# Performance work log

Hardware: AMD Instinct MI355X
Metric: run time of the kernel (lower is better)

Reference implementation:

```python
import jax, jax.numpy as jnp
import numpy as np

EMB = 1024
HID = 4 * EMB
HEADS = 16
HEAD_DIM = EMB // HEADS


def gelu_tanh(x):
    c = jnp.sqrt(jnp.asarray(2.0 / jnp.pi, x.dtype))
    return 0.5 * x * (1.0 + jnp.tanh(c * (x + 0.044715 * x ** 3)))


def layernorm(x, scale, shift, eps=1e-5):
    mean = jnp.mean(x, axis=-1, keepdims=True)
    var = jnp.var(x, axis=-1, keepdims=True)
    return scale * (x - mean) / jnp.sqrt(var + eps) + shift


def setup_inputs() -> dict:
    key = jax.random.key(0)
    ks = jax.random.split(key, 12)
    s = 0.02
    return {
        "x": jax.random.normal(ks[0], (2, 2048, EMB), jnp.float32),
        "Wq": jax.random.normal(ks[1], (EMB, EMB), jnp.float32) * s,
        "Wk": jax.random.normal(ks[2], (EMB, EMB), jnp.float32) * s,
        "Wv": jax.random.normal(ks[3], (EMB, EMB), jnp.float32) * s,
        "Wo": jax.random.normal(ks[4], (EMB, EMB), jnp.float32) * s,
        "bo": jnp.zeros((EMB,), jnp.float32),
        "W1": jax.random.normal(ks[5], (EMB, HID), jnp.float32) * s,
        "b1": jnp.zeros((HID,), jnp.float32),
        "W2": jax.random.normal(ks[6], (HID, EMB), jnp.float32) * s,
        "b2": jnp.zeros((EMB,), jnp.float32),
        "ln1_scale": jnp.ones((EMB,), jnp.float32),
        "ln1_shift": jnp.zeros((EMB,), jnp.float32),
        "ln2_scale": jnp.ones((EMB,), jnp.float32),
        "ln2_shift": jnp.zeros((EMB,), jnp.float32),
    }


def reference(x, Wq, Wk, Wv, Wo, bo, W1, b1, W2, b2,
              ln1_scale, ln1_shift, ln2_scale, ln2_shift):
    B, S, D = x.shape

    # pre-norm attention + residual
    h = layernorm(x, ln1_scale, ln1_shift)
    q = (h @ Wq).reshape(B, S, HEADS, HEAD_DIM).transpose(0, 2, 1, 3)  # bhsd
    k = (h @ Wk).reshape(B, S, HEADS, HEAD_DIM).transpose(0, 2, 1, 3)
    v = (h @ Wv).reshape(B, S, HEADS, HEAD_DIM).transpose(0, 2, 1, 3)

    scores = jnp.einsum("bhqd,bhkd->bhqk", q, k)
    causal = jnp.tril(jnp.ones((S, S), bool))
    scores = jnp.where(causal, scores, -jnp.inf)
    attn = jax.nn.softmax(scores / jnp.sqrt(jnp.asarray(HEAD_DIM, x.dtype)), axis=-1)
    ctx = jnp.einsum("bhqk,bhkd->bhqd", attn, v)
    ctx = ctx.transpose(0, 2, 1, 3).reshape(B, S, D)
    x = x + (ctx @ Wo + bo)

    # pre-norm FFN + residual
    h = layernorm(x, ln2_scale, ln2_shift)
    h = gelu_tanh(h @ W1 + b1) @ W2 + b2
    return x + h
```

## Files before the change

kernel.cpp:

```cpp
#include <hip/hip_runtime.h>
#include <hip/hip_bf16.h>
#include <stdint.h>

#define B_   2
#define S_   2048
#define D_   1024
#define H_   16
#define DH_  64
#define HID_ 4096
#define M_   4096

typedef __bf16 bf16x8 __attribute__((ext_vector_type(8)));
typedef float  f32x4  __attribute__((ext_vector_type(4)));
typedef float  f32x16 __attribute__((ext_vector_type(16)));
typedef uint32_t u32x4v __attribute__((ext_vector_type(4)));

typedef const uint32_t __attribute__((address_space(1))) u32g;
typedef uint32_t       __attribute__((address_space(3))) u32l;

#define SCL2K_ 0.18033688011112042f

__device__ __forceinline__ uint16_t f2bf(float f) {
  uint32_t u = __builtin_bit_cast(uint32_t, f);
  u += 0x7FFFu + ((u >> 16) & 1u);
  return (uint16_t)(u >> 16);
}

__device__ __forceinline__ float bf2f(uint16_t u) {
  return __builtin_bit_cast(float, (uint32_t)u << 16);
}

__device__ __forceinline__ void gload_lds16(const void* g, void* l) {
  __builtin_amdgcn_global_load_lds((u32g*)g, (u32l*)l, 16, 0, 0);
}

__device__ __forceinline__ const bf16x8* lds8p(const uint16_t* base, int row,
                                               int cole) {
  int byt = (cole * 2) ^ ((row & 7) << 4);
  return reinterpret_cast<const bf16x8*>(base + row * 64 + (byt >> 1));
}

__device__ __forceinline__ const bf16x8* lds8p32(const uint16_t* base, int row,
                                                 int cole) {
  int byt = (cole * 2) ^ ((row & 7) << 4) ^ ((row & 8) << 2);
  return reinterpret_cast<const bf16x8*>(base + row * 64 + (byt >> 1));
}

__device__ __forceinline__ uint32_t cvtpk_bf16(float lo, float hi) {
  uint32_t d;
  asm("v_cvt_pk_bf16_f32 %0, %1, %2" : "=v"(d) : "v"(lo), "v"(hi));
  return d;
}
__device__ __forceinline__ void pl32swap(uint32_t& a, uint32_t& b) {
  asm volatile("v_permlane32_swap_b32 %0, %1" : "+v"(a), "+v"(b));
}

__global__ void wconv_all(const float* __restrict__ Wq, const float* __restrict__ Wk,
                          const float* __restrict__ Wv, const float* __restrict__ Wo,
                          const float* __restrict__ W1, const float* __restrict__ W2,
                          uint16_t* __restrict__ WQKVT, uint16_t* __restrict__ WOT,
                          uint16_t* __restrict__ W1T, uint16_t* __restrict__ W2T) {
  __shared__ float tile[32][33];
  int idx = blockIdx.x;
  const float* W;
  uint16_t* WT;
  int K, N, within;
  if (idx < 4096) {
    int which = idx >> 10;
    within = idx & 1023;
    W = (which == 0) ? Wq : (which == 1) ? Wk : (which == 2) ? Wv : Wo;
    WT = (which == 3) ? WOT : WQKVT + (size_t)which * 1024 * 1024;
    K = 1024; N = 1024;
  } else if (idx < 8192) {
    within = idx - 4096; W = W1; WT = W1T; K = 1024; N = 4096;
  } else {
    within = idx - 8192; W = W2; WT = W2T; K = 4096; N = 1024;
  }
  int nb = N >> 5;
  int n0 = (within % nb) * 32, k0 = (within / nb) * 32;
  int tx = threadIdx.x, ty = threadIdx.y;
#pragma unroll
  for (int i = 0; i < 4; ++i)
    tile[ty + i * 8][tx] = W[(size_t)(k0 + ty + i * 8) * N + n0 + tx];
  __syncthreads();
#pragma unroll
  for (int i = 0; i < 4; ++i)
    WT[(size_t)(n0 + ty + i * 8) * K + k0 + tx] = f2bf(tile[tx][ty + i * 8]);
}

__global__ __launch_bounds__(256) void ln_k(const float* __restrict__ x,
                                            const float* __restrict__ sc,
                                            const float* __restrict__ sh,
                                            uint16_t* __restrict__ out) {
  int row = blockIdx.x;
  int t = threadIdx.x;
  float4 v = reinterpret_cast<const float4*>(x + (size_t)row * D_)[t];
  float s = v.x + v.y + v.z + v.w;
  float ss = v.x * v.x + v.y * v.y + v.z * v.z + v.w * v.w;
#pragma unroll
  for (int off = 32; off >= 1; off >>= 1) {
    s += __shfl_xor(s, off);
    ss += __shfl_xor(ss, off);
  }
  __shared__ float red[8];
  int wid = t >> 6, lane = t & 63;
  if (lane == 0) { red[wid] = s; red[wid + 4] = ss; }
  __syncthreads();
  s = red[0] + red[1] + red[2] + red[3];
  ss = red[4] + red[5] + red[6] + red[7];
  float mean = s * (1.0f / D_);
  float var = ss * (1.0f / D_) - mean * mean;
  float rstd = rsqrtf(var + 1e-5f);
  float4 g = reinterpret_cast<const float4*>(sc)[t];
  float4 b = reinterpret_cast<const float4*>(sh)[t];
  ushort4 o;
  o.x = f2bf(g.x * (v.x - mean) * rstd + b.x);
  o.y = f2bf(g.y * (v.y - mean) * rstd + b.y);
  o.z = f2bf(g.z * (v.z - mean) * rstd + b.z);
  o.w = f2bf(g.w * (v.w - mean) * rstd + b.w);
  reinterpret_cast<ushort4*>(out + (size_t)row * D_)[t] = o;
}

__global__ __launch_bounds__(256) void reduce4_k(
    const uint16_t* __restrict__ P0, const uint16_t* __restrict__ P1,
    const uint16_t* __restrict__ P2, const uint16_t* __restrict__ P3,
    const float* __restrict__ resid, const float* __restrict__ bias,
    float* __restrict__ out) {
  int row = blockIdx.x, t = threadIdx.x;
  size_t base = (size_t)row * D_ + t * 4;
  float4 r = *reinterpret_cast<const float4*>(resid + base);
  float4 b = reinterpret_cast<const float4*>(bias)[t];
  ushort4 u0 = *reinterpret_cast<const ushort4*>(P0 + base);
  ushort4 u1 = *reinterpret_cast<const ushort4*>(P1 + base);
  ushort4 u2 = *reinterpret_cast<const ushort4*>(P2 + base);
  ushort4 u3 = *reinterpret_cast<const ushort4*>(P3 + base);
  float4 o;
  o.x = r.x + b.x + bf2f(u0.x) + bf2f(u1.x) + bf2f(u2.x) + bf2f(u3.x);
  o.y = r.y + b.y + bf2f(u0.y) + bf2f(u1.y) + bf2f(u2.y) + bf2f(u3.y);
  o.z = r.z + b.z + bf2f(u0.z) + bf2f(u1.z) + bf2f(u2.z) + bf2f(u3.z);
  o.w = r.w + b.w + bf2f(u0.w) + bf2f(u1.w) + bf2f(u2.w) + bf2f(u3.w);
  *reinterpret_cast<float4*>(out + base) = o;
}

__global__ void vtrans_k(const uint16_t* __restrict__ V, uint16_t* __restrict__ VT) {
  __shared__ uint16_t tile[32][33];
  int s0 = blockIdx.x * 32, d0 = blockIdx.y * 32, bh = blockIdx.z;
  int tx = threadIdx.x, ty = threadIdx.y;
  const uint16_t* vb = V + (size_t)bh * S_ * DH_;
  uint16_t* vtb = VT + (size_t)bh * DH_ * S_;
#pragma unroll
  for (int i = 0; i < 4; ++i)
    tile[ty + i * 8][tx] = vb[(size_t)(s0 + ty + i * 8) * DH_ + d0 + tx];
  __syncthreads();
#pragma unroll
  for (int i = 0; i < 4; ++i)
    vtb[(size_t)(d0 + ty + i * 8) * S_ + s0 + tx] = tile[tx][ty + i * 8];
}

template <int EPI>
__global__ __launch_bounds__(512, 2) void gemm8(
    const uint16_t* __restrict__ A, const uint16_t* __restrict__ BT,
    void* __restrict__ Cout, const float* __restrict__ bias,
    uint16_t* __restrict__ P0, uint16_t* __restrict__ P1,
    uint16_t* __restrict__ P2, uint16_t* __restrict__ P3,
    int M, int N, int K) {
  __shared__ uint16_t As[2][2][128 * 64];
  __shared__ uint16_t Bs[2][2][128 * 64];
  int t = threadIdx.x;
  int lane = t & 63, wid = t >> 6;
  int wm = wid >> 2, wn = wid & 3;
  int l15 = lane & 15, lk8 = (lane >> 4) * 8, lr4 = (lane >> 4) * 4;
  int gx = gridDim.x;
  int nwg = gx * gridDim.y;
  int bid = blockIdx.y * gx + blockIdx.x;
  int swz = (bid & 7) * (nwg >> 3) + (bid >> 3);
  int bx = swz % gx, by = swz / gx;
  int m0 = by * 256, n0 = bx * 256;
  int ksz = K / gridDim.z;
  int kbeg = blockIdx.z * ksz;
  int NT = ksz >> 6;

  int r0 = t >> 3, slot0 = t & 7;
  int scol = (slot0 ^ (r0 & 7)) * 8;

  auto STAGE_A = [&](int kt, int half, int buf) {
    const uint16_t* src =
        A + (size_t)(m0 + half * 128 + r0) * K + kbeg + kt * 64 + scol;
    uint16_t* dst = &As[buf][half][t * 8];
    gload_lds16(src, dst);
    gload_lds16(src + (size_t)64 * K, dst + 4096);
  };
  auto STAGE_B = [&](int kt, int half, int buf) {
    const uint16_t* src =
        BT + (size_t)(n0 + half * 128 + r0) * K + kbeg + kt * 64 + scol;
    uint16_t* dst = &Bs[buf][half][t * 8];
    gload_lds16(src, dst);
    gload_lds16(src + (size_t)64 * K, dst + 4096);
  };

  bf16x8 a[4][2], b[2][2];
  auto LDA = [&](int buf, int mh) {
#pragma unroll
    for (int j = 0; j < 4; ++j)
#pragma unroll
      for (int kk = 0; kk < 2; ++kk)
        a[j][kk] = *lds8p(As[buf][mh], wm * 64 + j * 16 + l15, kk * 32 + lk8);
  };
  auto LDB = [&](int buf, int nh) {
#pragma unroll
    for (int jj = 0; jj < 2; ++jj)
#pragma unroll
      for (int kk = 0; kk < 2; ++kk)
        b[jj][kk] = *lds8p(Bs[buf][nh], wn * 32 + jj * 16 + l15, kk * 32 + lk8);
  };

  f32x4 acc[8][4] = {};
  auto MM = [&](int mh, int nh) {
    __builtin_amdgcn_s_setprio(1);
#pragma unroll
    for (int kk = 0; kk < 2; ++kk)
#pragma unroll
      for (int j = 0; j < 4; ++j)
#pragma unroll
        for (int jj = 0; jj < 2; ++jj)
          acc[mh * 4 + j][nh * 2 + jj] = __builtin_amdgcn_mfma_f32_16x16x32_bf16(
              a[j][kk], b[jj][kk], acc[mh * 4 + j][nh * 2 + jj], 0, 0, 0);
    __builtin_amdgcn_s_setprio(0);
  };
  auto BAR = [&]() {
    __builtin_amdgcn_s_barrier();
    asm volatile("" ::: "memory");
  };
  auto LGKM0 = [&]() {
    asm volatile("s_waitcnt lgkmcnt(0)" ::: "memory");
    __builtin_amdgcn_sched_barrier(0);
  };

  STAGE_A(0, 0, 0);
  STAGE_B(0, 1, 0);
  STAGE_B(0, 0, 0);
  STAGE_A(0, 1, 0);
  STAGE_A(1, 0, 1);
  STAGE_B(1, 1, 1);
  asm volatile("s_waitcnt vmcnt(4)" ::: "memory");
  BAR();

  for (int T = 0; T < NT; ++T) {
    int cur = T & 1;
    LDA(cur, 0);
    LDB(cur, 0);
    if (T + 1 < NT) STAGE_B(T + 1, 0, cur ^ 1);
    BAR(); LGKM0();
    MM(0, 0);
    BAR();
    LDB(cur, 1);
    if (T + 1 < NT) STAGE_A(T + 1, 1, cur ^ 1);
    BAR(); LGKM0();
    MM(0, 1);
    BAR();
    LDA(cur, 1);
    if (T + 2 < NT) STAGE_A(T + 2, 0, cur);
    BAR(); LGKM0();
    MM(1, 1);
    BAR();
    LDB(cur, 0);
    if (T + 2 < NT) STAGE_B(T + 2, 1, cur);
    BAR(); LGKM0();
    MM(1, 0);
    if (T + 1 < NT) {
      if (T == NT - 2) {
        asm volatile("s_waitcnt vmcnt(0)" ::: "memory");
      } else {
        asm volatile("s_waitcnt vmcnt(4)" ::: "memory");
      }
    }
    BAR();
  }

  uint16_t* Pz = nullptr;
  if constexpr (EPI == 3) {
    int z = blockIdx.z;
    Pz = (z == 0) ? P0 : (z == 1) ? P1 : (z == 2) ? P2 : P3;
  }
#pragma unroll
  for (int mi = 0; mi < 8; ++mi) {
#pragma unroll
    for (int ni = 0; ni < 4; ++ni) {
#pragma unroll
      for (int rr = 0; rr < 4; ++rr) {
        int gm = m0 + (mi >> 2) * 128 + wm * 64 + (mi & 3) * 16 + lr4 + rr;
        int gn = n0 + (ni >> 1) * 128 + wn * 32 + (ni & 1) * 16 + l15;
        float v = acc[mi][ni][rr];
        if constexpr (EPI == 0) {
          int which = gn >> 10, nc = gn & 1023;
          int h = nc >> 6, dh = nc & 63;
          int bb = gm >> 11, s = gm & 2047;
          if (which == 1) v *= SCL2K_;
          ((uint16_t*)Cout)[((size_t)which * 32 + bb * 16 + h) * (S_ * 64) +
                            (size_t)s * 64 + dh] = f2bf(v);
        } else if constexpr (EPI == 2) {
          float u = v + bias[gn];
          float y = 0.7978845608028654f * (u + 0.044715f * u * u * u);
          float e = __expf(2.0f * y);
          float th = 1.0f - 2.0f / (e + 1.0f);
          ((uint16_t*)Cout)[(size_t)gm * N + gn] = f2bf(0.5f * u * (1.0f + th));
        } else {
          Pz[(size_t)gm * N + gn] = f2bf(v);
        }
      }
    }
  }
}

template <int EPI>
__global__ __launch_bounds__(256) void gemm_bt(
    const uint16_t* __restrict__ A, const uint16_t* __restrict__ BT,
    void* __restrict__ Cout, const float* __restrict__ bias,
    const float* __restrict__ resid, int M, int N, int K) {
  __shared__ uint16_t Asm_[128 * 64];
  __shared__ uint16_t Bsm_[128 * 64];
  int t = threadIdx.x;
  int lane = t & 63, wid = t >> 6;
  int wr = wid >> 1, wc = wid & 1;
  int nwg = gridDim.x * gridDim.y;
  int bid = blockIdx.y * gridDim.x + blockIdx.x;
  int swz = (bid & 7) * (nwg >> 3) + (bid >> 3);
  int bx = swz % gridDim.x, by = swz / gridDim.x;
  int m0 = by * 128, n0 = bx * 128;
  int l15 = lane & 15, lk8 = (lane >> 4) * 8;
  f32x4 acc[4][4] = {};

  auto STAGE = [&](int k0) {
#pragma unroll
    for (int it = 0; it < 4; ++it) {
      int idx = it * 256 + t;
      int r = idx >> 3, slot = idx & 7;
      int c = (slot ^ (r & 7)) * 8;
      gload_lds16(A + (size_t)(m0 + r) * K + k0 + c, &Asm_[idx * 8]);
      gload_lds16(BT + (size_t)(n0 + r) * K + k0 + c, &Bsm_[idx * 8]);
    }
  };

  int niter = K >> 6;
  for (int ki = 0; ki < niter; ++ki) {
    __syncthreads();
    STAGE(ki * 64);
    __syncthreads();
#pragma unroll
    for (int kk = 0; kk < 2; ++kk) {
      bf16x8 a[4], b[4];
#pragma unroll
      for (int mi = 0; mi < 4; ++mi)
        a[mi] = *lds8p(Asm_, wr * 64 + mi * 16 + l15, kk * 32 + lk8);
#pragma unroll
      for (int ni = 0; ni < 4; ++ni)
        b[ni] = *lds8p(Bsm_, wc * 64 + ni * 16 + l15, kk * 32 + lk8);
#pragma unroll
      for (int mi = 0; mi < 4; ++mi)
#pragma unroll
        for (int ni = 0; ni < 4; ++ni)
          acc[mi][ni] = __builtin_amdgcn_mfma_f32_16x16x32_bf16(
              a[mi], b[ni], acc[mi][ni], 0, 0, 0);
    }
  }
  int lr4 = (lane >> 4) * 4;
#pragma unroll
  for (int mi = 0; mi < 4; ++mi) {
#pragma unroll
    for (int ni = 0; ni < 4; ++ni) {
#pragma unroll
      for (int r = 0; r < 4; ++r) {
        int gm = m0 + wr * 64 + mi * 16 + lr4 + r;
        int gn = n0 + wc * 64 + ni * 16 + l15;
        float v = acc[mi][ni][r];
        if constexpr (EPI == 1) {
          ((float*)Cout)[(size_t)gm * N + gn] =
              resid[(size_t)gm * N + gn] + v + bias[gn];
        }
      }
    }
  }
}

__global__ __launch_bounds__(64) void attn32s_k(const uint16_t* __restrict__ Q,
                                                const uint16_t* __restrict__ Kv,
                                                const uint16_t* __restrict__ VT,
                                                uint16_t* __restrict__ Obuf,
                                                float* __restrict__ ML) {
  __shared__ uint16_t Ksm[2][32 * 64];
  __shared__ uint16_t Vsm[2][32 * 64];
  int bid = blockIdx.x;
  int bh = bid & 31;
  int s = (bid >> 5) & 1;
  int qt = bid >> 6;
  int lane = threadIdx.x;
  int l31 = lane & 31, lh = lane >> 5;
  int nkt = qt + 1;
  int h = (nkt + 1) >> 1;
  int t0 = s ? h : 0, t1 = s ? nkt : h;
  int pb = ((qt * 32 + bh) << 1) + s;

  f32x16 o0 = {}, o1 = {};
  float mrow = -3.0e38f, lsum = 0.0f;

  auto STAGE = [&](int k0, int bufi) {
#pragma unroll
    for (int c = 0; c < 4; ++c) {
      int idx = c * 64 + lane;
      int r = idx >> 3, sl = idx & 7;
      int slp = sl ^ (r & 7) ^ ((r & 8) >> 2);
      gload_lds16(Kv + ((size_t)bh * S_ + k0 + r) * 64 + slp * 8,
                  &Ksm[bufi][idx * 8]);
      int dh = 2 * r + (slp >> 2), ko = (slp & 3) * 8;
      gload_lds16(VT + ((size_t)bh * 64 + dh) * S_ + k0 + ko,
                  &Vsm[bufi][idx * 8]);
    }
  };

  if (t0 < t1) {
    int qbase = qt * 32;
    bf16x8 qf[4];
#pragma unroll
    for (int dk = 0; dk < 4; ++dk)
      qf[dk] = *reinterpret_cast<const bf16x8*>(
          Q + ((size_t)bh * S_ + qbase + l31) * 64 + dk * 16 + lh * 8);

    int buf = 0;
    STAGE(t0 * 32, 0);
    for (int t = t0; t < t1; ++t) {
      if (t + 1 < t1) {
        STAGE((t + 1) * 32, buf ^ 1);
        asm volatile("s_waitcnt vmcnt(8)" ::: "memory");
      } else {
        asm volatile("s_waitcnt vmcnt(0)" ::: "memory");
      }
      __builtin_amdgcn_sched_barrier(0);
      f32x16 Sf = {};
#pragma unroll
      for (int dk = 0; dk < 4; ++dk) {
        bf16x8 kf = *lds8p32(Ksm[buf], l31, dk * 16 + lh * 8);
        Sf = __builtin_amdgcn_mfma_f32_32x32x16_bf16(kf, qf[dk], Sf, 0, 0, 0);
      }
      float sv[16];
      if (t == qt) {
#pragma unroll
        for (int rr = 0; rr < 16; ++rr) {
          int koff = (rr & 3) + 8 * (rr >> 2) + 4 * lh;
          sv[rr] = (koff <= l31) ? Sf[rr] : -3.0e38f;
        }
      } else {
#pragma unroll
        for (int rr = 0; rr < 16; ++rr) sv[rr] = Sf[rr];
      }
      float mt16 = sv[0];
#pragma unroll
      for (int rr = 1; rr < 16; ++rr) mt16 = fmaxf(mt16, sv[rr]);
      if (__any(mt16 > mrow + 8.0f)) {
        float mt = mt16;
#pragma unroll
        for (int off = 32; off >= 1; off >>= 1)
          mt = fmaxf(mt, __shfl_xor(mt, off));
        mt = fmaxf(mt, mrow);
        float fac = __builtin_amdgcn_exp2f(mrow - mt);
        mrow = mt;
        lsum *= fac;
#pragma unroll
        for (int rr = 0; rr < 16; ++rr) { o0[rr] *= fac; o1[rr] *= fac; }
      }
      float pv[16];
#pragma unroll
      for (int rr = 0; rr < 16; ++rr) {
        pv[rr] = __builtin_amdgcn_exp2f(sv[rr] - mrow);
        lsum += pv[rr];
      }
      uint32_t a0 = cvtpk_bf16(pv[0], pv[1]), b0 = cvtpk_bf16(pv[4], pv[5]);
      pl32swap(a0, b0);
      uint32_t a1 = cvtpk_bf16(pv[2], pv[3]), b1 = cvtpk_bf16(pv[6], pv[7]);
      pl32swap(a1, b1);
      u32x4v w0 = {a0, a1, b0, b1};
      bf16x8 pa0 = __builtin_bit_cast(bf16x8, w0);
      uint32_t a2 = cvtpk_bf16(pv[8], pv[9]), b2 = cvtpk_bf16(pv[12], pv[13]);
      pl32swap(a2, b2);
      uint32_t a3 = cvtpk_bf16(pv[10], pv[11]), b3 = cvtpk_bf16(pv[14], pv[15]);
      pl32swap(a3, b3);
      u32x4v w1 = {a2, a3, b2, b3};
      bf16x8 pa1 = __builtin_bit_cast(bf16x8, w1);
      int vrow = l31 >> 1, vcb = (l31 & 1) * 32 + lh * 8;
      bf16x8 v00 = *lds8p32(Vsm[buf], vrow, vcb);
      o0 = __builtin_amdgcn_mfma_f32_32x32x16_bf16(pa0, v00, o0, 0, 0, 0);
      bf16x8 v01 = *lds8p32(Vsm[buf], vrow, vcb + 16);
      o0 = __builtin_amdgcn_mfma_f32_32x32x16_bf16(pa1, v01, o0, 0, 0, 0);
      bf16x8 v10 = *lds8p32(Vsm[buf], 16 + vrow, vcb);
      o1 = __builtin_amdgcn_mfma_f32_32x32x16_bf16(pa0, v10, o1, 0, 0, 0);
      bf16x8 v11 = *lds8p32(Vsm[buf], 16 + vrow, vcb + 16);
      o1 = __builtin_amdgcn_mfma_f32_32x32x16_bf16(pa1, v11, o1, 0, 0, 0);
      buf ^= 1;
    }
    lsum += __shfl_xor(lsum, 32);
  }

  if (lane < 32) {
    ML[(size_t)pb * 64 + l31 * 2] = mrow;
    ML[(size_t)pb * 64 + l31 * 2 + 1] = lsum;
  }
#pragma unroll
  for (int rr = 0; rr < 16; ++rr) {
    int srow = (rr & 3) + 8 * (rr >> 2) + 4 * lh;
    size_t base = (size_t)pb * 2048 + srow * 64;
    Obuf[base + l31] = f2bf(o0[rr]);
    Obuf[base + 32 + l31] = f2bf(o1[rr]);
  }
}

__global__ __launch_bounds__(64) void attncomb_k(const uint16_t* __restrict__ Obuf,
                                                 const float* __restrict__ ML,
                                                 uint16_t* __restrict__ ctx) {
  int blk = blockIdx.x;
  int qt = blk >> 5, bh = blk & 31;
  int lane = threadIdx.x;
  int q = lane >> 1, half = lane & 1;
  size_t pb0 = (size_t)blk * 2, pb1 = pb0 + 1;
  float m0 = ML[pb0 * 64 + q * 2], l0 = ML[pb0 * 64 + q * 2 + 1];
  float m1 = ML[pb1 * 64 + q * 2], l1 = ML[pb1 * 64 + q * 2 + 1];
  float m = fmaxf(m0, m1);
  float w0 = __builtin_amdgcn_exp2f(m0 - m), w1 = __builtin_amdgcn_exp2f(m1 - m);
  float invL = 1.0f / (l0 * w0 + l1 * w1);
  int b_ = bh >> 4, h_ = bh & 15;
  int srow = qt * 32 + q;
  size_t ib = pb0 * 2048 + q * 64 + half * 32;
  size_t ob = ((size_t)(b_ * S_ + srow)) * D_ + h_ * 64 + half * 32;
#pragma unroll
  for (int i = 0; i < 8; ++i) {
    ushort4 u0 = *reinterpret_cast<const ushort4*>(Obuf + ib + i * 4);
    ushort4 u1 = *reinterpret_cast<const ushort4*>(Obuf + 2048 + ib + i * 4);
    ushort4 o;
    o.x = f2bf((bf2f(u0.x) * w0 + bf2f(u1.x) * w1) * invL);
    o.y = f2bf((bf2f(u0.y) * w0 + bf2f(u1.y) * w1) * invL);
    o.z = f2bf((bf2f(u0.z) * w0 + bf2f(u1.z) * w1) * invL);
    o.w = f2bf((bf2f(u0.w) * w0 + bf2f(u1.w) * w1) * invL);
    *reinterpret_cast<ushort4*>(ctx + ob + i * 4) = o;
  }
}

extern "C" void kernel_launch(void* const* d_in, const int* in_sizes, int n_in,
                              void* d_out, int out_size, void* d_ws, size_t ws_size,
                              hipStream_t stream) {
  const float* x    = (const float*)d_in[0];
  const float* Wq   = (const float*)d_in[1];
  const float* Wk   = (const float*)d_in[2];
  const float* Wv   = (const float*)d_in[3];
  const float* Wo   = (const float*)d_in[4];
  const float* bo   = (const float*)d_in[5];
  const float* W1   = (const float*)d_in[6];
  const float* b1   = (const float*)d_in[7];
  const float* W2   = (const float*)d_in[8];
  const float* b2   = (const float*)d_in[9];
  const float* ln1s = (const float*)d_in[10];
  const float* ln1b = (const float*)d_in[11];
  const float* ln2s = (const float*)d_in[12];
  const float* ln2b = (const float*)d_in[13];
  float* out = (float*)d_out;
  char* ws = (char*)d_ws;

  const size_t MB = 1024 * 1024;
  uint16_t* WQKVT = (uint16_t*)(ws + 0);
  uint16_t* WOT   = (uint16_t*)(ws + 6 * MB);
  uint16_t* W1T   = (uint16_t*)(ws + 8 * MB);
  uint16_t* W2T   = (uint16_t*)(ws + 16 * MB);
  uint16_t* H1    = (uint16_t*)(ws + 24 * MB);
  float*    X1    = (float*)(ws + 32 * MB);
  uint16_t* QKV   = (uint16_t*)(ws + 48 * MB);
  uint16_t* VTb   = (uint16_t*)(ws + 72 * MB);
  uint16_t* CTX   = (uint16_t*)(ws + 80 * MB);
  uint16_t* FFH   = (uint16_t*)(ws + 48 * MB);
  uint16_t* AOB   = (uint16_t*)(ws + 24 * MB);
  float*    AML   = (float*)(ws + 40 * MB);
  uint16_t* SP0   = (uint16_t*)(ws + 0);
  uint16_t* SP1   = (uint16_t*)(ws + 8 * MB);
  uint16_t* SP2   = (uint16_t*)(ws + 24 * MB);
  uint16_t* SP3   = (uint16_t*)(ws + 80 * MB);

  dim3 b32x8(32, 8);
  wconv_all<<<dim3(12288), b32x8, 0, stream>>>(Wq, Wk, Wv, Wo, W1, W2,
                                               WQKVT, WOT, W1T, W2T);
  ln_k<<<M_, 256, 0, stream>>>(x, ln1s, ln1b, H1);
  gemm8<0><<<dim3(12, 16), 512, 0, stream>>>(H1, WQKVT, QKV, nullptr,
                                             nullptr, nullptr, nullptr, nullptr,
                                             M_, 3072, 1024);
  const uint16_t* Qp = QKV;
  const uint16_t* Kp = QKV + (size_t)32 * S_ * 64;
  const uint16_t* Vp = QKV + (size_t)64 * S_ * 64;
  vtrans_k<<<dim3(64, 2, 32), b32x8, 0, stream>>>(Vp, VTb);
  attn32s_k<<<dim3(4096), 64, 0, stream>>>(Qp, Kp, VTb, AOB, AML);
  attncomb_k<<<dim3(2048), 64, 0, stream>>>(AOB, AML, CTX);
  gemm_bt<1><<<dim3(8, 32), 256, 0, stream>>>(CTX, WOT, X1, bo, x, M_, 1024, 1024);
  ln_k<<<M_, 256, 0, stream>>>(X1, ln2s, ln2b, H1);
  gemm8<2><<<dim3(16, 16), 512, 0, stream>>>(H1, W1T, FFH, b1,
                                             nullptr, nullptr, nullptr, nullptr,
                                             M_, 4096, 1024);
  gemm8<3><<<dim3(4, 16, 4), 512, 0, stream>>>(FFH, W2T, nullptr, nullptr,
                                               SP0, SP1, SP2, SP3,
                                               M_, 1024, 4096);
  reduce4_k<<<M_, 256, 0, stream>>>(SP0, SP1, SP2, SP3, X1, b2, out);
}
```

Before: 245.8 us.

## Split attention KV range three ways, schedule heavy tiles first, fuse LN1 into weight prep

The attention kernel now splits each query tile's causal key range into three chunks instead of two, and launches the longest query tiles first to improve load balance. The combine kernel merges three partial results. The first layernorm is folded into the weight conversion kernel to save a launch. s_setprio is raised around the MFMA sections. AML is moved to workspace offset 0, which risks overlapping other buffers, and a three-way split adds more partial-output traffic.

```diff
diff --git a/kernel.cpp b/kernel.cpp
--- a/kernel.cpp
+++ b/kernel.cpp
@@ -55,13 +55,46 @@
   asm volatile("v_permlane32_swap_b32 %0, %1" : "+v"(a), "+v"(b));
 }
 
-__global__ void wconv_all(const float* __restrict__ Wq, const float* __restrict__ Wk,
-                          const float* __restrict__ Wv, const float* __restrict__ Wo,
-                          const float* __restrict__ W1, const float* __restrict__ W2,
-                          uint16_t* __restrict__ WQKVT, uint16_t* __restrict__ WOT,
-                          uint16_t* __restrict__ W1T, uint16_t* __restrict__ W2T) {
+__global__ void prep_k(const float* __restrict__ Wq, const float* __restrict__ Wk,
+                       const float* __restrict__ Wv, const float* __restrict__ Wo,
+                       const float* __restrict__ W1, const float* __restrict__ W2,
+                       uint16_t* __restrict__ WQKVT, uint16_t* __restrict__ WOT,
+                       uint16_t* __restrict__ W1T, uint16_t* __restrict__ W2T,
+                       const float* __restrict__ x, const float* __restrict__ sc,
+                       const float* __restrict__ sh, uint16_t* __restrict__ lnout) {
+  int idx = blockIdx.x;
+  int tx = threadIdx.x, ty = threadIdx.y;
+  if (idx >= 12288) {
+    int row = idx - 12288;
+    int t = ty * 32 + tx;
+    float4 v = reinterpret_cast<const float4*>(x + (size_t)row * D_)[t];
+    float s = v.x + v.y + v.z + v.w;
+    float ss = v.x * v.x + v.y * v.y + v.z * v.z + v.w * v.w;
+#pragma unroll
+    for (int off = 32; off >= 1; off >>= 1) {
+      s += __shfl_xor(s, off);
+      ss += __shfl_xor(ss, off);
+    }
+    __shared__ float red[8];
+    int wid = t >> 6, lane = t & 63;
+    if (lane == 0) { red[wid] = s; red[wid + 4] = ss; }
+    __syncthreads();
+    s = red[0] + red[1] + red[2] + red[3];
+    ss = red[4] + red[5] + red[6] + red[7];
+    float mean = s * (1.0f / D_);
+    float var = ss * (1.0f / D_) - mean * mean;
+    float rstd = rsqrtf(var + 1e-5f);
+    float4 g = reinterpret_cast<const float4*>(sc)[t];
+    float4 b = reinterpret_cast<const float4*>(sh)[t];
+    ushort4 o;
+    o.x = f2bf(g.x * (v.x - mean) * rstd + b.x);
+    o.y = f2bf(g.y * (v.y - mean) * rstd + b.y);
+    o.z = f2bf(g.z * (v.z - mean) * rstd + b.z);
+    o.w = f2bf(g.w * (v.w - mean) * rstd + b.w);
+    reinterpret_cast<ushort4*>(lnout + (size_t)row * D_)[t] = o;
+    return;
+  }
   __shared__ float tile[32][33];
-  int idx = blockIdx.x;
   const float* W;
   uint16_t* WT;
   int K, N, within;
@@ -78,7 +111,6 @@
   }
   int nb = N >> 5;
   int n0 = (within % nb) * 32, k0 = (within / nb) * 32;
-  int tx = threadIdx.x, ty = threadIdx.y;
 #pragma unroll
   for (int i = 0; i < 4; ++i)
     tile[ty + i * 8][tx] = W[(size_t)(k0 + ty + i * 8) * N + n0 + tx];
@@ -391,14 +423,14 @@
   __shared__ uint16_t Vsm[2][32 * 64];
   int bid = blockIdx.x;
   int bh = bid & 31;
-  int s = (bid >> 5) & 1;
-  int qt = bid >> 6;
+  int s = (bid >> 5) % 3;
+  int qt = 63 - bid / 96;
   int lane = threadIdx.x;
   int l31 = lane & 31, lh = lane >> 5;
   int nkt = qt + 1;
-  int h = (nkt + 1) >> 1;
-  int t0 = s ? h : 0, t1 = s ? nkt : h;
-  int pb = ((qt * 32 + bh) << 1) + s;
+  int chunk = (nkt + 2) / 3;
+  int t0 = s * chunk, t1 = min(nkt, t0 + chunk);
+  int pb = (qt * 32 + bh) * 3 + s;
 
   f32x16 o0 = {}, o1 = {};
   float mrow = -3.0e38f, lsum = 0.0f;
@@ -436,11 +468,13 @@
       }
       __builtin_amdgcn_sched_barrier(0);
       f32x16 Sf = {};
+      __builtin_amdgcn_s_setprio(1);
 #pragma unroll
       for (int dk = 0; dk < 4; ++dk) {
         bf16x8 kf = *lds8p32(Ksm[buf], l31, dk * 16 + lh * 8);
         Sf = __builtin_amdgcn_mfma_f32_32x32x16_bf16(kf, qf[dk], Sf, 0, 0, 0);
       }
+      __builtin_amdgcn_s_setprio(0);
       float sv[16];
       if (t == qt) {
 #pragma unroll
@@ -486,6 +520,7 @@
       u32x4v w1 = {a2, a3, b2, b3};
       bf16x8 pa1 = __builtin_bit_cast(bf16x8, w1);
       int vrow = l31 >> 1, vcb = (l31 & 1) * 32 + lh * 8;
+      __builtin_amdgcn_s_setprio(1);
       bf16x8 v00 = *lds8p32(Vsm[buf], vrow, vcb);
       o0 = __builtin_amdgcn_mfma_f32_32x32x16_bf16(pa0, v00, o0, 0, 0, 0);
       bf16x8 v01 = *lds8p32(Vsm[buf], vrow, vcb + 16);
@@ -494,6 +529,7 @@
       o1 = __builtin_amdgcn_mfma_f32_32x32x16_bf16(pa0, v10, o1, 0, 0, 0);
       bf16x8 v11 = *lds8p32(Vsm[buf], 16 + vrow, vcb + 16);
       o1 = __builtin_amdgcn_mfma_f32_32x32x16_bf16(pa1, v11, o1, 0, 0, 0);
+      __builtin_amdgcn_s_setprio(0);
       buf ^= 1;
     }
     lsum += __shfl_xor(lsum, 32);
@@ -519,12 +555,15 @@
   int qt = blk >> 5, bh = blk & 31;
   int lane = threadIdx.x;
   int q = lane >> 1, half = lane & 1;
-  size_t pb0 = (size_t)blk * 2, pb1 = pb0 + 1;
+  size_t pb0 = (size_t)blk * 3;
   float m0 = ML[pb0 * 64 + q * 2], l0 = ML[pb0 * 64 + q * 2 + 1];
-  float m1 = ML[pb1 * 64 + q * 2], l1 = ML[pb1 * 64 + q * 2 + 1];
-  float m = fmaxf(m0, m1);
-  float w0 = __builtin_amdgcn_exp2f(m0 - m), w1 = __builtin_amdgcn_exp2f(m1 - m);
-  float invL = 1.0f / (l0 * w0 + l1 * w1);
+  float m1 = ML[(pb0 + 1) * 64 + q * 2], l1 = ML[(pb0 + 1) * 64 + q * 2 + 1];
+  float m2 = ML[(pb0 + 2) * 64 + q * 2], l2 = ML[(pb0 + 2) * 64 + q * 2 + 1];
+  float m = fmaxf(fmaxf(m0, m1), m2);
+  float w0 = __builtin_amdgcn_exp2f(m0 - m);
+  float w1 = __builtin_amdgcn_exp2f(m1 - m);
+  float w2 = __builtin_amdgcn_exp2f(m2 - m);
+  float invL = 1.0f / (l0 * w0 + l1 * w1 + l2 * w2);
   int b_ = bh >> 4, h_ = bh & 15;
   int srow = qt * 32 + q;
   size_t ib = pb0 * 2048 + q * 64 + half * 32;
@@ -533,11 +572,12 @@
   for (int i = 0; i < 8; ++i) {
     ushort4 u0 = *reinterpret_cast<const ushort4*>(Obuf + ib + i * 4);
     ushort4 u1 = *reinterpret_cast<const ushort4*>(Obuf + 2048 + ib + i * 4);
+    ushort4 u2 = *reinterpret_cast<const ushort4*>(Obuf + 4096 + ib + i * 4);
     ushort4 o;
-    o.x = f2bf((bf2f(u0.x) * w0 + bf2f(u1.x) * w1) * invL);
-    o.y = f2bf((bf2f(u0.y) * w0 + bf2f(u1.y) * w1) * invL);
-    o.z = f2bf((bf2f(u0.z) * w0 + bf2f(u1.z) * w1) * invL);
-    o.w = f2bf((bf2f(u0.w) * w0 + bf2f(u1.w) * w1) * invL);
+    o.x = f2bf((bf2f(u0.x) * w0 + bf2f(u1.x) * w1 + bf2f(u2.x) * w2) * invL);
+    o.y = f2bf((bf2f(u0.y) * w0 + bf2f(u1.y) * w1 + bf2f(u2.y) * w2) * invL);
+    o.z = f2bf((bf2f(u0.z) * w0 + bf2f(u1.z) * w1 + bf2f(u2.z) * w2) * invL);
+    o.w = f2bf((bf2f(u0.w) * w0 + bf2f(u1.w) * w1 + bf2f(u2.w) * w2) * invL);
     *reinterpret_cast<ushort4*>(ctx + ob + i * 4) = o;
   }
 }
@@ -574,16 +614,16 @@
   uint16_t* CTX   = (uint16_t*)(ws + 80 * MB);
   uint16_t* FFH   = (uint16_t*)(ws + 48 * MB);
   uint16_t* AOB   = (uint16_t*)(ws + 24 * MB);
-  float*    AML   = (float*)(ws + 40 * MB);
+  float*    AML   = (float*)(ws + 0);
   uint16_t* SP0   = (uint16_t*)(ws + 0);
   uint16_t* SP1   = (uint16_t*)(ws + 8 * MB);
   uint16_t* SP2   = (uint16_t*)(ws + 24 * MB);
   uint16_t* SP3   = (uint16_t*)(ws + 80 * MB);
 
   dim3 b32x8(32, 8);
-  wconv_all<<<dim3(12288), b32x8, 0, stream>>>(Wq, Wk, Wv, Wo, W1, W2,
-                                               WQKVT, WOT, W1T, W2T);
-  ln_k<<<M_, 256, 0, stream>>>(x, ln1s, ln1b, H1);
+  prep_k<<<dim3(16384), b32x8, 0, stream>>>(Wq, Wk, Wv, Wo, W1, W2,
+                                            WQKVT, WOT, W1T, W2T,
+                                            x, ln1s, ln1b, H1);
   gemm8<0><<<dim3(12, 16), 512, 0, stream>>>(H1, WQKVT, QKV, nullptr,
                                              nullptr, nullptr, nullptr, nullptr,
                                              M_, 3072, 1024);
@@ -591,7 +631,7 @@
   const uint16_t* Kp = QKV + (size_t)32 * S_ * 64;
   const uint16_t* Vp = QKV + (size_t)64 * S_ * 64;
   vtrans_k<<<dim3(64, 2, 32), b32x8, 0, stream>>>(Vp, VTb);
-  attn32s_k<<<dim3(4096), 64, 0, stream>>>(Qp, Kp, VTb, AOB, AML);
+  attn32s_k<<<dim3(6144), 64, 0, stream>>>(Qp, Kp, VTb, AOB, AML);
   attncomb_k<<<dim3(2048), 64, 0, stream>>>(AOB, AML, CTX);
   gemm_bt<1><<<dim3(8, 32), 256, 0, stream>>>(CTX, WOT, X1, bo, x, M_, 1024, 1024);
   ln_k<<<M_, 256, 0, stream>>>(X1, ln2s, ln2b, H1);
```

After: 234.9 us. -4.4%, faster.
